# Kernel optimization log

Measured on AMD Instinct MI355X. Metric: run time of the kernel, lower is better.

The kernel has to match this reference:

```python
import jax, jax.numpy as jnp
import numpy as np

B, T, C = 2, 2048, 1024
N_HEAD = 16
HEAD_DIM = C // N_HEAD  # 64


def _apply_rope(x, inv_freq):
    # x: [B, H, T, hd]. Matches the torch module's mixed RoPE variant:
    # cos/sin built from cat(freqs, freqs) but x split by even/odd strides.
    Tn, hd = x.shape[2], x.shape[3]
    t = jnp.arange(Tn, dtype=inv_freq.dtype)
    freqs = t[:, None] * inv_freq[None, :]            # [T, hd/2]
    emb = jnp.concatenate([freqs, freqs], axis=-1)    # [T, hd]
    cos = jnp.cos(emb)[None, None, :, :]
    sin = jnp.sin(emb)[None, None, :, :]
    x1 = x[..., 0::2]
    x2 = x[..., 1::2]
    # interleave (-x2, x1) back to last dim: stack then flatten last two dims
    x_rot = jnp.stack((-x2, x1), axis=-1).reshape(x.shape)
    return x * cos + x_rot * sin


def setup_inputs() -> dict:
    key = jax.random.key(0)
    k1, k2, k3 = jax.random.split(key, 3)
    x = jax.random.normal(k1, (B, T, C), dtype=jnp.float32)
    w_qkv = jax.random.normal(k2, (C, 3 * C), dtype=jnp.float32) * 0.02
    w_proj = jax.random.normal(k3, (C, C), dtype=jnp.float32) * 0.02
    return {"x": x, "w_qkv": w_qkv, "w_proj": w_proj}


def reference(x, w_qkv, w_proj):
    Bn, Tn, Cn = x.shape
    hd = HEAD_DIM
    inv_freq = 1.0 / (10000.0 ** (jnp.arange(0, hd, 2, dtype=jnp.float32) / hd))

    qkv = jnp.einsum('btc,cd->btd', x, w_qkv)  # [B, T, 3C]
    q, k, v = jnp.split(qkv, 3, axis=2)
    # [B, T, C] -> [B, H, T, hd]
    q = q.reshape(Bn, Tn, N_HEAD, hd).transpose(0, 2, 1, 3)
    k = k.reshape(Bn, Tn, N_HEAD, hd).transpose(0, 2, 1, 3)
    v = v.reshape(Bn, Tn, N_HEAD, hd).transpose(0, 2, 1, 3)

    q = _apply_rope(q, inv_freq)
    k = _apply_rope(k, inv_freq)

    scale = 1.0 / jnp.sqrt(jnp.asarray(hd, dtype=q.dtype))
    scores = jnp.einsum('bhqd,bhkd->bhqk', q, k) * scale  # [B, H, T, T]
    causal = jnp.tril(jnp.ones((Tn, Tn), dtype=bool))
    scores = jnp.where(causal[None, None, :, :], scores, -jnp.inf)
    attn = jax.nn.softmax(scores, axis=-1)
    out = jnp.einsum('bhqk,bhkd->bhqd', attn, v)          # [B, H, T, hd]
    y = out.transpose(0, 2, 1, 3).reshape(Bn, Tn, Cn)     # [B, T, C]
    return jnp.einsum('btc,cd->btd', y, w_proj)
```

## Files before the change

### kernel.cpp

```cpp
#include <hip/hip_runtime.h>
#include <hip/hip_bf16.h>

typedef unsigned short u16;
typedef unsigned int u32;
typedef __attribute__((ext_vector_type(8))) __bf16 bf16x8;
typedef __attribute__((ext_vector_type(4))) float f32x4;
typedef __attribute__((ext_vector_type(4))) u16 u16x4;
typedef __attribute__((ext_vector_type(8))) u16 u16x8;
typedef __attribute__((ext_vector_type(4))) u32 u32x4;

__device__ __forceinline__ u16 f2bf(float f) {
  return __builtin_bit_cast(u16, (__bf16)f);
}

__device__ __forceinline__ void gload_lds16(const void* g, void* l) {
  __builtin_amdgcn_global_load_lds((const __attribute__((address_space(1))) void*)g,
                                   (__attribute__((address_space(3))) void*)l, 16, 0, 0);
}

__global__ __launch_bounds__(256) void prep_kernel(const float* __restrict__ x, u16* __restrict__ xb,
                                                   const float* __restrict__ wq, u16* __restrict__ wqT,
                                                   const float* __restrict__ wp, u16* __restrict__ wpT) {
  const int bid = blockIdx.x;
  const int tid = threadIdx.x;
  if (bid < 4096) {
    const int i = (bid * 256 + tid) * 4;
    const float4 v = *(const float4*)(x + i);
    u16x4 r = {f2bf(v.x), f2bf(v.y), f2bf(v.z), f2bf(v.w)};
    *(u16x4*)(xb + i) = r;
    return;
  }
  __shared__ u16 tile[64][65];
  const float* w;
  u16* wt;
  int K, N, n0, k0;
  if (bid < 4864) {
    const int id = bid - 4096;
    w = wq; wt = wqT; K = 1024; N = 3072;
    n0 = (id % 48) * 64; k0 = (id / 48) * 64;
  } else {
    const int id = bid - 4864;
    w = wp; wt = wpT; K = 1024; N = 1024;
    n0 = (id % 16) * 64; k0 = (id / 16) * 64;
  }
#pragma unroll
  for (int it = 0; it < 16; ++it) {
    const int idx = it * 256 + tid;
    const int r = idx >> 6, c = idx & 63;
    tile[r][c] = f2bf(w[(size_t)(k0 + r) * N + n0 + c]);
  }
  __syncthreads();
#pragma unroll
  for (int it = 0; it < 16; ++it) {
    const int idx = it * 256 + tid;
    const int r2 = idx >> 6, c2 = idx & 63;
    wt[(size_t)(n0 + r2) * K + k0 + c2] = tile[c2][r2];
  }
}

template <int BM, int MODE>
__global__ __launch_bounds__(256) void gemm_bt(const u16* __restrict__ A, const u16* __restrict__ Bt,
                                               void* __restrict__ Cout, int M, int N, int K,
                                               u16* __restrict__ Qo, u16* __restrict__ Ko,
                                               u16* __restrict__ Vto) {
  constexpr int MR = (BM == 128) ? 4 : 2;
  constexpr int SMEM_U16 = BM * 64 + 8192;
  __shared__ __align__(16) u16 smem[SMEM_U16];
  u16* As0 = smem;
  u16* As1 = smem + BM * 32;
  u16* Bs0 = smem + BM * 64;
  u16* Bs1 = smem + BM * 64 + 4096;
  const int tid = threadIdx.x;
  const int wave = tid >> 6;
  const int lane = tid & 63;
  const int la = lane & 15, lb = lane >> 4;
  const int nwg = gridDim.x * gridDim.y;
  int lid = blockIdx.y * gridDim.x + blockIdx.x;
  lid = (lid & 7) * (nwg >> 3) + (lid >> 3);
  const int m0 = (lid % gridDim.x) * BM, n0 = (lid / gridDim.x) * 128;
  const int wr = (wave >> 1) * (BM / 2), wc = (wave & 1) * 64;
  const int srow = lane >> 2;
  const int scol = (lane & 3) * 8;
  const int c0 = wave * 2;

  auto stage = [&](int bb, int k0) {
    u16* Asb = bb ? As1 : As0;
    u16* Bsb = bb ? Bs1 : Bs0;
    if (BM == 128) {
#pragma unroll
      for (int c2 = 0; c2 < 2; ++c2) {
        const int c = c0 + c2;
        const int row = c * 16 + srow;
        gload_lds16(A + (size_t)(m0 + row) * K + k0 + scol, Asb + c * 512);
      }
    } else {
      const int row = wave * 16 + srow;
      gload_lds16(A + (size_t)(m0 + row) * K + k0 + scol, Asb + wave * 512);
    }
#pragma unroll
    for (int c2 = 0; c2 < 2; ++c2) {
      const int c = c0 + c2;
      const int row = c * 16 + srow;
      gload_lds16(Bt + (size_t)(n0 + row) * K + k0 + scol, Bsb + c * 512);
    }
  };

  f32x4 acc[MR][4] = {};
  const int nk = K >> 5;
  stage(0, 0);
  __syncthreads();
  int cur = 0;
  for (int t = 0; t < nk; ++t) {
    if (t + 1 < nk) stage(cur ^ 1, (t + 1) * 32);
    const u16* Asc = cur ? As1 : As0;
    const u16* Bsc = cur ? Bs1 : Bs0;
    bf16x8 af[MR], bfr[4];
#pragma unroll
    for (int m = 0; m < MR; ++m) af[m] = *(const bf16x8*)&Asc[(wr + m * 16 + la) * 32 + lb * 8];
#pragma unroll
    for (int n = 0; n < 4; ++n) bfr[n] = *(const bf16x8*)&Bsc[(wc + n * 16 + la) * 32 + lb * 8];
#pragma unroll
    for (int m = 0; m < MR; ++m)
#pragma unroll
      for (int n = 0; n < 4; ++n)
        acc[m][n] = __builtin_amdgcn_mfma_f32_16x16x32_bf16(af[m], bfr[n], acc[m][n], 0, 0, 0);
    __syncthreads();
    cur ^= 1;
  }

  if (MODE == 2) {
    const int reg = n0 >> 10;
    if (reg == 2) {
#pragma unroll
      for (int n = 0; n < 4; ++n) {
        const int cl = wc + n * 16 + la;
#pragma unroll
        for (int m = 0; m < MR; ++m)
#pragma unroll
          for (int j = 0; j < 4; ++j) {
            const int row = wr + m * 16 + lb * 4 + j;
            smem[cl * 128 + (row ^ ((cl & 7) << 3))] = f2bf(acc[m][n][j]);
          }
      }
      __syncthreads();
      const int bb = m0 >> 11;
      const int tbase = m0 & 2047;
      const int h0 = (n0 & 1023) >> 6;
#pragma unroll
      for (int it = 0; it < 8; ++it) {
        const int cl = it * 16 + (tid >> 4);
        const int tch = tid & 15;
        const u16x8 v = *(const u16x8*)&smem[cl * 128 + ((tch * 8) ^ ((cl & 7) << 3))];
        const int d = cl & 63;
        const int h = h0 + (cl >> 6);
        *(u16x8*)(Vto + ((size_t)(bb * 16 + h) * 64 + d) * 2048 + tbase + tch * 8) = v;
      }
      return;
    }
    const float NEG = -0.41524101186f;
    const float QSC = 0.18033688011f;
    u16* dst = (reg == 0) ? Qo : Ko;
    const float qs = (reg == 0) ? QSC : 1.0f;
    const int tb = m0 + wr + lb * 4;
    const int bb = tb >> 11;
    const int tlb = tb & 2047;
    const float sgn = (la & 1) ? 1.0f : -1.0f;
    float c1[2], s1[2], c16[2], s16[2], cm0[2], sm0[2];
#pragma unroll
    for (int p = 0; p < 2; ++p) {
      const float invf = exp2f(NEG * (float)((wc + p * 16 + la) & 31));
      sincosf(invf, &s1[p], &c1[p]);
      sincosf(16.0f * invf, &s16[p], &c16[p]);
      sincosf((float)tlb * invf, &sm0[p], &cm0[p]);
    }
#pragma unroll
    for (int n = 0; n < 4; ++n) {
      const int p = n & 1;
      const int cl = wc + n * 16 + la;
      const int d = cl & 63;
      const int h = ((n0 & 1023) >> 6) + (cl >> 6);
      const size_t plane = (size_t)(bb * 16 + h) * 2048;
      float cm = cm0[p], sm = sm0[p];
#pragma unroll
      for (int m = 0; m < MR; ++m) {
        float cj = cm, sj = sm;
#pragma unroll
        for (int j = 0; j < 4; ++j) {
          const float val = acc[m][n][j];
          const float prt = __shfl_xor(val, 1);
          const float out = (val * cj + sgn * prt * sj) * qs;
          dst[(plane + tlb + m * 16 + j) * 64 + d] = f2bf(out);
          const float cn = cj * c1[p] - sj * s1[p], sn = sj * c1[p] + cj * s1[p];
          cj = cn; sj = sn;
        }
        const float cn = cm * c16[p] - sm * s16[p], sn = sm * c16[p] + cm * s16[p];
        cm = cn; sm = sn;
      }
    }
    return;
  }

#pragma unroll
  for (int m = 0; m < MR; ++m)
#pragma unroll
    for (int n = 0; n < 4; ++n)
#pragma unroll
      for (int j = 0; j < 4; ++j) {
        const int row = m0 + wr + m * 16 + lb * 4 + j;
        const int col = n0 + wc + n * 16 + la;
        if (MODE == 1)
          ((float*)Cout)[(size_t)row * N + col] = acc[m][n][j];
        else
          ((u16*)Cout)[(size_t)row * N + col] = f2bf(acc[m][n][j]);
      }
}

__global__ __launch_bounds__(256) void attn_kernel(const u16* __restrict__ Q, const u16* __restrict__ K,
                                                   const u16* __restrict__ Vt, u16* __restrict__ Y) {
  const int L = blockIdx.y * 32 + blockIdx.x;
  const int xcd = L & 7, slot = L >> 3;
  const int bh = xcd * 4 + (slot & 3);
  const int beta = 31 - (slot >> 2);
  const int b = bh >> 4, h = bh & 15;
  const int wave = threadIdx.x >> 6, lane = threadIdx.x & 63;
  const int la = lane & 15, lb = lane >> 4;
  const int q0 = beta * 64 + wave * 16;
  const int NT = beta + 1;

  __shared__ __align__(16) u16 KV[2][2][4096];

  const size_t plane = (size_t)bh * (2048 * 64);
  const char* Kb = (const char*)(K + plane);
  const char* Vb = (const char*)(Vt + plane);

  auto stage = [&](int buf, int kt) {
#pragma unroll
    for (int it = 0; it < 2; ++it) {
      const int ci = it * 256 + wave * 64 + lane;
      const int row = ci >> 3;
      const int cbs = ((ci & 7) * 16) ^ ((row & 7) << 4);
      const int n2 = row >> 4, rho = row & 15;
      const int srow = ((n2 & 1) << 5) + ((rho >> 2) << 3) + ((n2 >> 1) << 2) + (rho & 3);
      gload_lds16(Kb + (size_t)(kt * 64 + srow) * 128 + cbs,
                  (char*)&KV[buf][0][0] + it * 4096 + wave * 1024);
      gload_lds16(Vb + (size_t)row * 4096 + (size_t)kt * 128 + cbs,
                  (char*)&KV[buf][1][0] + it * 4096 + wave * 1024);
    }
  };

  stage(0, 0);

  bf16x8 qf[2];
#pragma unroll
  for (int s = 0; s < 2; ++s)
    qf[s] = *(const bf16x8*)(Q + plane + (size_t)(q0 + la) * 64 + s * 32 + lb * 8);

  f32x4 o[4] = {};
  float mreg = -1.0e30f;
  float plr = 0.f;

  const int x0 = (la & 7) << 4;
  const int cu0 = ((lb * 16) ^ x0) >> 1;
  const int cu1 = ((64 + lb * 16) ^ x0) >> 1;

  __syncthreads();
  int buf = 0;
  for (int kt = 0; kt < NT; ++kt) {
    if (kt + 1 < NT) stage(buf ^ 1, kt + 1);
    const u16* Kc = KV[buf][0];
    const u16* Vc = KV[buf][1];

    bf16x8 kf[2][4];
#pragma unroll
    for (int n = 0; n < 4; ++n) {
      kf[0][n] = *(const bf16x8*)&Kc[(n * 16 + la) * 64 + cu0];
      kf[1][n] = *(const bf16x8*)&Kc[(n * 16 + la) * 64 + cu1];
    }

    const int rowq = q0 + la;
    f32x4 sa[4] = {};
    __builtin_amdgcn_s_setprio(1);
#pragma unroll
    for (int s = 0; s < 2; ++s)
#pragma unroll
      for (int n = 0; n < 4; ++n)
        sa[n] = __builtin_amdgcn_mfma_f32_16x16x32_bf16(kf[s][n], qf[s], sa[n], 0, 0, 0);
    __builtin_amdgcn_s_setprio(0);
    if (kt == NT - 1) {
#pragma unroll
      for (int n = 0; n < 4; ++n)
#pragma unroll
        for (int j = 0; j < 4; ++j) {
          const int col = kt * 64 + ((n & 1) << 5) + (lb << 3) + ((n >> 1) << 2) + j;
          if (col > rowq) sa[n][j] = -1.0e30f;
        }
    }
    float mn_[4];
#pragma unroll
    for (int n = 0; n < 4; ++n)
      mn_[n] = fmaxf(fmaxf(sa[n][0], sa[n][1]), fmaxf(sa[n][2], sa[n][3]));
    const float lmax = fmaxf(fmaxf(mn_[0], mn_[1]), fmaxf(mn_[2], mn_[3]));
    if (__any(lmax > mreg + 8.0f)) {
      float v = fmaxf(lmax, __shfl_xor(lmax, 16));
      v = fmaxf(v, __shfl_xor(v, 32));
      const float mn = fmaxf(mreg, v);
      const float al = __builtin_amdgcn_exp2f(mreg - mn);
      plr *= al;
      mreg = mn;
      float alj[4];
#pragma unroll
      for (int j = 0; j < 4; ++j) alj[j] = __shfl(al, lb * 4 + j);
#pragma unroll
      for (int n = 0; n < 4; ++n)
#pragma unroll
        for (int j = 0; j < 4; ++j) o[n][j] *= alj[j];
    }
    u32 w[4][2];
    float ps = 0.f;
#pragma unroll
    for (int n = 0; n < 4; ++n) {
      const float p0 = __builtin_amdgcn_exp2f(sa[n][0] - mreg);
      const float p1 = __builtin_amdgcn_exp2f(sa[n][1] - mreg);
      const float p2 = __builtin_amdgcn_exp2f(sa[n][2] - mreg);
      const float p3 = __builtin_amdgcn_exp2f(sa[n][3] - mreg);
      ps += (p0 + p1) + (p2 + p3);
      w[n][0] = (u32)f2bf(p0) | ((u32)f2bf(p1) << 16);
      w[n][1] = (u32)f2bf(p2) | ((u32)f2bf(p3) << 16);
    }
    plr += ps;
    bf16x8 paf[2];
    paf[0] = __builtin_bit_cast(bf16x8, (u32x4){w[0][0], w[0][1], w[2][0], w[2][1]});
    paf[1] = __builtin_bit_cast(bf16x8, (u32x4){w[1][0], w[1][1], w[3][0], w[3][1]});

    bf16x8 vf[2][4];
#pragma unroll
    for (int n = 0; n < 4; ++n) {
      vf[0][n] = *(const bf16x8*)&Vc[(n * 16 + la) * 64 + cu0];
      vf[1][n] = *(const bf16x8*)&Vc[(n * 16 + la) * 64 + cu1];
    }
    __builtin_amdgcn_s_setprio(1);
#pragma unroll
    for (int n = 0; n < 4; ++n)
#pragma unroll
      for (int s = 0; s < 2; ++s)
        o[n] = __builtin_amdgcn_mfma_f32_16x16x32_bf16(paf[s], vf[s][n], o[n], 0, 0, 0);
    __builtin_amdgcn_s_setprio(0);

    __syncthreads();
    buf ^= 1;
  }

  float ls = plr;
  ls += __shfl_xor(ls, 16);
  ls += __shfl_xor(ls, 32);
  const float rinv = __builtin_amdgcn_rcpf(ls);
  float rj[4];
#pragma unroll
  for (int j = 0; j < 4; ++j) rj[j] = __shfl(rinv, lb * 4 + j);
#pragma unroll
  for (int n = 0; n < 4; ++n)
#pragma unroll
    for (int j = 0; j < 4; ++j) {
      const int t = q0 + lb * 4 + j;
      const int c = h * 64 + n * 16 + la;
      Y[((size_t)b * 2048 + t) * 1024 + c] = f2bf(o[n][j] * rj[j]);
    }
}

extern "C" void kernel_launch(void* const* d_in, const int* in_sizes, int n_in, void* d_out,
                              int out_size, void* d_ws, size_t ws_size, hipStream_t stream) {
  (void)in_sizes; (void)n_in; (void)out_size; (void)ws_size;
  const float* x = (const float*)d_in[0];
  const float* w_qkv = (const float*)d_in[1];
  const float* w_proj = (const float*)d_in[2];
  char* ws = (char*)d_ws;
  u16* xb     = (u16*)(ws);
  u16* wqkvT  = (u16*)(ws + 8388608);
  u16* wprojT = (u16*)(ws + 14680064);
  u16* q      = (u16*)(ws + 16777216);
  u16* k      = (u16*)(ws + 25165824);
  u16* vt     = (u16*)(ws + 33554432);
  u16* y      = xb;

  prep_kernel<<<dim3(5120), dim3(256), 0, stream>>>(x, xb, w_qkv, wqkvT, w_proj, wprojT);
  gemm_bt<128, 2><<<dim3(32, 24), dim3(256), 0, stream>>>(xb, wqkvT, nullptr, 4096, 3072, 1024,
                                                          q, k, vt);
  attn_kernel<<<dim3(32, 32), dim3(256), 0, stream>>>(q, k, vt, y);
  gemm_bt<64, 1><<<dim3(64, 8), dim3(256), 0, stream>>>(y, wprojT, d_out, 4096, 1024, 1024,
                                                        nullptr, nullptr, nullptr);
}
```

Baseline: 112.6 us.

## Precompute RoPE cos/sin table and stage Q/K epilogue through LDS for vector stores

The prep kernel now also fills a global [T,32] table of (cos, sin) pairs, so the QKV GEMM epilogue reads rotation factors instead of doing sincos and recurrence rotations per thread. The Q/K epilogue also writes the rotated results into a swizzled LDS tile and then issues coalesced 16-byte global stores, replacing scattered 2-byte stores. This adds table traffic and an extra barrier. It also reuses the GEMM's LDS buffer, which must be large enough for a 128x128 tile.

```diff
diff --git a/kernel.cpp b/kernel.cpp
--- a/kernel.cpp
+++ b/kernel.cpp
@@ -20,7 +20,8 @@
 
 __global__ __launch_bounds__(256) void prep_kernel(const float* __restrict__ x, u16* __restrict__ xb,
                                                    const float* __restrict__ wq, u16* __restrict__ wqT,
-                                                   const float* __restrict__ wp, u16* __restrict__ wpT) {
+                                                   const float* __restrict__ wp, u16* __restrict__ wpT,
+                                                   float2* __restrict__ tbl) {
   const int bid = blockIdx.x;
   const int tid = threadIdx.x;
   if (bid < 4096) {
@@ -28,6 +29,16 @@
     const float4 v = *(const float4*)(x + i);
     u16x4 r = {f2bf(v.x), f2bf(v.y), f2bf(v.z), f2bf(v.w)};
     *(u16x4*)(xb + i) = r;
+    return;
+  }
+  if (bid >= 5120) {
+    const float NEG = -0.41524101186f;
+    const int e = (bid - 5120) * 256 + tid;
+    const int t = e >> 5, i = e & 31;
+    const float ang = (float)t * exp2f(NEG * (float)i);
+    float s, c;
+    sincosf(ang, &s, &c);
+    tbl[e] = make_float2(c, s);
     return;
   }
   __shared__ u16 tile[64][65];
@@ -62,7 +73,7 @@
 __global__ __launch_bounds__(256) void gemm_bt(const u16* __restrict__ A, const u16* __restrict__ Bt,
                                                void* __restrict__ Cout, int M, int N, int K,
                                                u16* __restrict__ Qo, u16* __restrict__ Ko,
-                                               u16* __restrict__ Vto) {
+                                               u16* __restrict__ Vto, const float2* __restrict__ Tb) {
   constexpr int MR = (BM == 128) ? 4 : 2;
   constexpr int SMEM_U16 = BM * 64 + 8192;
   __shared__ __align__(16) u16 smem[SMEM_U16];
@@ -130,6 +141,9 @@
 
   if (MODE == 2) {
     const int reg = n0 >> 10;
+    const int bb = m0 >> 11;
+    const int tbase = m0 & 2047;
+    const int h0 = (n0 & 1023) >> 6;
     if (reg == 2) {
 #pragma unroll
       for (int n = 0; n < 4; ++n) {
@@ -143,9 +157,6 @@
           }
       }
       __syncthreads();
-      const int bb = m0 >> 11;
-      const int tbase = m0 & 2047;
-      const int h0 = (n0 & 1023) >> 6;
 #pragma unroll
       for (int it = 0; it < 8; ++it) {
         const int cl = it * 16 + (tid >> 4);
@@ -157,45 +168,46 @@
       }
       return;
     }
-    const float NEG = -0.41524101186f;
     const float QSC = 0.18033688011f;
     u16* dst = (reg == 0) ? Qo : Ko;
     const float qs = (reg == 0) ? QSC : 1.0f;
-    const int tb = m0 + wr + lb * 4;
-    const int bb = tb >> 11;
-    const int tlb = tb & 2047;
     const float sgn = (la & 1) ? 1.0f : -1.0f;
-    float c1[2], s1[2], c16[2], s16[2], cm0[2], sm0[2];
-#pragma unroll
-    for (int p = 0; p < 2; ++p) {
-      const float invf = exp2f(NEG * (float)((wc + p * 16 + la) & 31));
-      sincosf(invf, &s1[p], &c1[p]);
-      sincosf(16.0f * invf, &s16[p], &c16[p]);
-      sincosf((float)tlb * invf, &sm0[p], &cm0[p]);
-    }
-#pragma unroll
-    for (int n = 0; n < 4; ++n) {
-      const int p = n & 1;
-      const int cl = wc + n * 16 + la;
-      const int d = cl & 63;
-      const int h = ((n0 & 1023) >> 6) + (cl >> 6);
-      const size_t plane = (size_t)(bb * 16 + h) * 2048;
-      float cm = cm0[p], sm = sm0[p];
-#pragma unroll
-      for (int m = 0; m < MR; ++m) {
-        float cj = cm, sj = sm;
+    const int i0 = (wc + la) & 31;
+    const int i1 = (wc + 16 + la) & 31;
+#pragma unroll
+    for (int m = 0; m < MR; ++m) {
+      const int rbase = wr + m * 16 + lb * 4;
+      float2 ct0[4], ct1[4];
+#pragma unroll
+      for (int j = 0; j < 4; ++j) {
+        const int t = tbase + rbase + j;
+        ct0[j] = Tb[t * 32 + i0];
+        ct1[j] = Tb[t * 32 + i1];
+      }
+#pragma unroll
+      for (int n = 0; n < 4; ++n) {
+        const int cl = wc + n * 16 + la;
 #pragma unroll
         for (int j = 0; j < 4; ++j) {
           const float val = acc[m][n][j];
           const float prt = __shfl_xor(val, 1);
-          const float out = (val * cj + sgn * prt * sj) * qs;
-          dst[(plane + tlb + m * 16 + j) * 64 + d] = f2bf(out);
-          const float cn = cj * c1[p] - sj * s1[p], sn = sj * c1[p] + cj * s1[p];
-          cj = cn; sj = sn;
+          const float c = (n & 1) ? ct1[j].x : ct0[j].x;
+          const float s = (n & 1) ? ct1[j].y : ct0[j].y;
+          const float out = (val * c + sgn * prt * s) * qs;
+          const int row = rbase + j;
+          smem[row * 128 + (cl ^ ((row & 7) << 3))] = f2bf(out);
         }
-        const float cn = cm * c16[p] - sm * s16[p], sn = sm * c16[p] + cm * s16[p];
-        cm = cn; sm = sn;
-      }
+      }
+    }
+    __syncthreads();
+#pragma unroll
+    for (int it = 0; it < 8; ++it) {
+      const int row = it * 16 + (tid >> 4);
+      const int tc = tid & 15;
+      const u16x8 v = *(const u16x8*)&smem[row * 128 + ((tc * 8) ^ ((row & 7) << 3))];
+      const int d = (tc * 8) & 63;
+      const int h = h0 + (tc >> 3);
+      *(u16x8*)(dst + ((size_t)(bb * 16 + h) * 2048 + tbase + row) * 64 + d) = v;
     }
     return;
   }
@@ -380,12 +392,13 @@
   u16* q      = (u16*)(ws + 16777216);
   u16* k      = (u16*)(ws + 25165824);
   u16* vt     = (u16*)(ws + 33554432);
+  float2* tbl = (float2*)(ws + 41943040);
   u16* y      = xb;
 
-  prep_kernel<<<dim3(5120), dim3(256), 0, stream>>>(x, xb, w_qkv, wqkvT, w_proj, wprojT);
+  prep_kernel<<<dim3(5376), dim3(256), 0, stream>>>(x, xb, w_qkv, wqkvT, w_proj, wprojT, tbl);
   gemm_bt<128, 2><<<dim3(32, 24), dim3(256), 0, stream>>>(xb, wqkvT, nullptr, 4096, 3072, 1024,
-                                                          q, k, vt);
+                                                          q, k, vt, tbl);
   attn_kernel<<<dim3(32, 32), dim3(256), 0, stream>>>(q, k, vt, y);
   gemm_bt<64, 1><<<dim3(64, 8), dim3(256), 0, stream>>>(y, wprojT, d_out, 4096, 1024, 1024,
-                                                        nullptr, nullptr, nullptr);
-}
+                                                        nullptr, nullptr, nullptr, nullptr);
+}
```

Measured after the change: 112.9 us. About the same (+0.3%).
